# Performance work log

Measured on AMD Instinct MI355X. Metric: run time of the kernel, lower is better.

## Reference

```python
import jax, jax.numpy as jnp
import numpy as np

N, D, K = 131072, 256, 16      # samples, ambient dim, projection dims
NDOM, B, G = 8, 32, 100        # domains, hist_bins, barycenter grid size


def setup_inputs() -> dict:
    key = jax.random.key(0)
    k1, k2, k3, k4, k5, k6 = jax.random.split(key, 6)
    X = jax.random.normal(k1, (N, D), jnp.float32)
    y = jax.random.randint(k2, (N,), 0, NDOM)
    # wT: orthonormal columns via QR with sign fix (as in INB.__init__)
    wi = np.asarray(jax.random.normal(k3, (D, K), jnp.float32))
    Q, R = np.linalg.qr(wi)
    wT = jnp.asarray(Q * np.sign(np.diag(R)), jnp.float32)
    # Per-(domain, dim) histogram bin edges (sorted -> monotone) and CDF values in [0,1]
    bin_edges = jnp.sort(jax.random.normal(k4, (NDOM, K, B + 1), jnp.float32) * 2.0, axis=-1)
    steps = jax.random.uniform(k5, (NDOM, K, B), jnp.float32, minval=0.1, maxval=1.0)
    c = jnp.cumsum(steps, axis=-1)
    cdf_vals = jnp.concatenate([jnp.zeros((NDOM, K, 1), jnp.float32), c / c[..., -1:]], axis=-1)
    # Barycenter inverse-CDF (quantile function) sampled on a uniform grid over [0,1]
    bary_q = jnp.sort(jax.random.normal(k6, (K, G), jnp.float32) * 2.0, axis=-1)
    return {"X": X, "y": y, "wT": wT, "bin_edges": bin_edges,
            "cdf_vals": cdf_vals, "bary_q": bary_q}


def _searchsorted_2d(edges, x):
    # edges: (N, K, B+1) per-sample monotone edges; x: (N, K)
    ss = jax.vmap(jax.vmap(lambda e, v: jnp.searchsorted(e, v, side='right')))(edges, x)
    return jnp.clip(ss - 1, 0, B - 1)  # (N, K) int, left bin index


def reference(X, y, wT, bin_edges, cdf_vals, bary_q):
    Xm = X @ wT                         # (N, K) small-K GEMM
    remaining = X - Xm @ wT.T           # (N, D)
    # gather per-sample domain tables (irregular, data-dependent access)
    eb = bin_edges[y]                   # (N, K, B+1)
    cb = cdf_vals[y]                    # (N, K, B+1)
    i = _searchsorted_2d(eb, Xm)        # (N, K)
    x0 = jnp.take_along_axis(eb, i[..., None], axis=-1)[..., 0]
    x1 = jnp.take_along_axis(eb, i[..., None] + 1, axis=-1)[..., 0]
    f0 = jnp.take_along_axis(cb, i[..., None], axis=-1)[..., 0]
    f1 = jnp.take_along_axis(cb, i[..., None] + 1, axis=-1)[..., 0]
    t = jnp.clip((Xm - x0) / (x1 - x0), 0.0, 1.0)
    u = f0 + t * (f1 - f0)              # per-domain CDF value in [0,1]
    # barycenter inverse CDF: linear interp on uniform grid over [0,1]
    pos = jnp.clip(u, 0.0, 1.0) * (G - 1)
    j = jnp.clip(pos.astype(jnp.int32), 0, G - 2)
    tt = pos - j.astype(pos.dtype)
    kk = jnp.arange(K)[None, :]
    z = bary_q[kk, j] * (1.0 - tt) + bary_q[kk, j + 1] * tt  # (N, K)
    return remaining + z @ wT.T
```

## Files before the change

kernel.cpp:

```cpp
#include <hip/hip_runtime.h>

typedef float v2f __attribute__((ext_vector_type(2)));
typedef float v4f __attribute__((ext_vector_type(4)));

#define N_ROWS 131072
#define DIM    256
#define KP     16
#define NDOM   8
#define NB     32
#define GG     100

#define EB_N   (NDOM*KP*(NB+1))
#define BARY_N (KP*GG)

#define GRID   1536
#define WAVES  4
#define NWAVE  (GRID*WAVES)
#define ITERS  22

__device__ __forceinline__ void pk_fma(v2f &d, v2f a, v2f b) {
    asm("v_pk_fma_f32 %0, %1, %2, %0" : "+v"(d) : "v"(a), "v"(b));
}
__device__ __forceinline__ void pl32swap(float &a, float &b) {
    asm("v_permlane32_swap_b32 %0, %1" : "+v"(a), "+v"(b));
}
__device__ __forceinline__ void pl16swap(float &a, float &b) {
    asm("v_permlane16_swap_b32 %0, %1" : "+v"(a), "+v"(b));
}
__device__ __forceinline__ v2f swap32_sum(v2f lo, v2f hi) {
    float a0 = lo[0], b0 = hi[0], a1 = lo[1], b1 = hi[1];
    pl32swap(a0, b0); pl32swap(a1, b1);
    v2f r; r[0] = a0 + b0; r[1] = a1 + b1; return r;
}
__device__ __forceinline__ v2f swap16_sum(v2f lo, v2f hi) {
    float a0 = lo[0], b0 = hi[0], a1 = lo[1], b1 = hi[1];
    pl16swap(a0, b0); pl16swap(a1, b1);
    v2f r; r[0] = a0 + b0; r[1] = a1 + b1; return r;
}
template <int CODE>
__device__ __forceinline__ float swzf(float x) {
    return __builtin_bit_cast(float,
        __builtin_amdgcn_ds_swizzle(__builtin_bit_cast(int, x), CODE));
}
template <int M>
__device__ __forceinline__ void xor_sum2(v2f &a, v2f &b) {
    constexpr int CODE = (M << 10) | 0x1F;
    a[0] += swzf<CODE>(a[0]); a[1] += swzf<CODE>(a[1]);
    b[0] += swzf<CODE>(b[0]); b[1] += swzf<CODE>(b[1]);
}
__device__ __forceinline__ void wave_fence() {
    asm volatile("s_waitcnt lgkmcnt(0)" ::: "memory");
    __builtin_amdgcn_sched_barrier(0);
}

__global__ __launch_bounds__(256, 4)
void inb_kernel(const float* __restrict__ X, const int* __restrict__ y,
                const float* __restrict__ wT, const float* __restrict__ be,
                const float* __restrict__ cv, const float* __restrict__ bq,
                float* __restrict__ out)
{
    __shared__ float sEB[EB_N];
    __shared__ float sBARY[BARY_N];
    __shared__ float sCOEFF[WAVES][16];

    const int tid = threadIdx.x;
    for (int i = tid; i < EB_N; i += 256) sEB[i] = be[i];
    for (int i = tid; i < BARY_N; i += 256) sBARY[i] = bq[i];
    __syncthreads();

    const int lane = tid & 63;
    const int wid  = tid >> 6;
    const int k      = ((lane & 48) >> 2) | (lane & 3);
    const int echunk = (lane >> 2) & 3;

    v2f wTo[4][8];
#pragma unroll
    for (int j = 0; j < 4; ++j) {
        const v4f* wrow = reinterpret_cast<const v4f*>(&wT[(4*lane + j)*KP]);
#pragma unroll
        for (int q = 0; q < 4; ++q) {
            v4f v = wrow[q];
            v2f a; a[0] = v[0]; a[1] = v[1]; wTo[j][2*q]   = a;
            v2f b; b[0] = v[2]; b[1] = v[3]; wTo[j][2*q+1] = b;
        }
    }

    float* cobuf = sCOEFF[wid];
    const int gwave = blockIdx.x * WAVES + wid;

    v4f x_cur = *reinterpret_cast<const v4f*>(&X[(size_t)gwave*DIM + 4*lane]);
    int pr1 = (gwave + NWAVE < N_ROWS) ? gwave + NWAVE : gwave;
    v4f x_nxt = *reinterpret_cast<const v4f*>(&X[(size_t)pr1*DIM + 4*lane]);
    int dom_cur = y[gwave];

    for (int it = 0; it < ITERS; ++it) {
        const int row = gwave + it*NWAVE;
        if (row >= N_ROWS) break;

        const float* ebRow = &sEB[(dom_cur*KP + k)*(NB+1)];
        float e[8];
#pragma unroll
        for (int t = 0; t < 8; ++t) e[t] = ebRow[8*echunk + t];

        int nr  = row + NWAVE;   if (nr  >= N_ROWS) nr  = row;
        int pfr = row + 2*NWAVE; if (pfr >= N_ROWS) pfr = row;
        int dom_nxt = y[nr];
        v4f x_pf = *reinterpret_cast<const v4f*>(&X[(size_t)pfr*DIM + 4*lane]);

        v2f P[8];
#pragma unroll
        for (int q = 0; q < 8; ++q) { P[q][0] = 0.f; P[q][1] = 0.f; }
#pragma unroll
        for (int j = 0; j < 4; ++j) {
            v2f xj; xj[0] = x_cur[j]; xj[1] = x_cur[j];
#pragma unroll
            for (int q = 0; q < 8; ++q) pk_fma(P[q], xj, wTo[j][q]);
        }

        v2f Q[4];
#pragma unroll
        for (int r = 0; r < 4; ++r)
            Q[r] = swap32_sum(P[r], P[r+4]);
        v2f S0 = swap16_sum(Q[0], Q[2]);
        v2f S1 = swap16_sum(Q[1], Q[3]);
        xor_sum2<8>(S0, S1);
        xor_sum2<4>(S0, S1);
        xor_sum2<2>(S0, S1);
        xor_sum2<1>(S0, S1);
        v2f T = (lane & 2) ? S1 : S0;
        const float xm = (lane & 1) ? T[1] : T[0];

        int cnt = (e[0] <= xm) + (e[1] <= xm) + (e[2] <= xm) + (e[3] <= xm)
                + (e[4] <= xm) + (e[5] <= xm) + (e[6] <= xm) + (e[7] <= xm);
        cnt += __builtin_amdgcn_ds_swizzle(cnt, 0x101F);
        cnt += __builtin_amdgcn_ds_swizzle(cnt, 0x201F);
        int i0 = min(max(cnt - 1, 0), NB - 1);

        float x0 = ebRow[i0], x1 = ebRow[i0+1];
        const float* cfRow = cv + (size_t)(dom_cur*KP + k)*(NB+1);
        float f0 = cfRow[i0], f1 = cfRow[i0+1];

        float t  = fminf(fmaxf(__fdividef(xm - x0, x1 - x0), 0.f), 1.f);
        float u  = f0 + t * (f1 - f0);
        float posv = fminf(fmaxf(u, 0.f), 1.f) * (float)(GG - 1);
        int jj = min((int)posv, GG - 2);
        float ttf = posv - (float)jj;
        float b0 = sBARY[k*GG + jj], b1 = sBARY[k*GG + jj + 1];
        float z = b0*(1.f - ttf) + b1*ttf;
        float coeff = xm - z;

        if ((lane & 12) == 0) cobuf[k] = coeff;
        wave_fence();

        v2f c2[8];
#pragma unroll
        for (int q = 0; q < 4; ++q) {
            v4f cv4 = *reinterpret_cast<const v4f*>(&cobuf[4*q]);
            v2f a; a[0] = cv4[0]; a[1] = cv4[1]; c2[2*q]   = a;
            v2f b; b[0] = cv4[2]; b[1] = cv4[3]; c2[2*q+1] = b;
        }
        float od[4];
#pragma unroll
        for (int j = 0; j < 4; ++j) {
            v2f a = {0.f,0.f};
#pragma unroll
            for (int q = 0; q < 8; ++q) pk_fma(a, c2[q], wTo[j][q]);
            od[j] = x_cur[j] - (a[0] + a[1]);
        }
        v4f o4; o4[0] = od[0]; o4[1] = od[1]; o4[2] = od[2]; o4[3] = od[3];
        *reinterpret_cast<v4f*>(&out[(size_t)row*DIM + 4*lane]) = o4;

        x_cur = x_nxt; x_nxt = x_pf; dom_cur = dom_nxt;
    }
}

extern "C" void kernel_launch(void* const* d_in, const int* in_sizes, int n_in,
                              void* d_out, int out_size, void* d_ws, size_t ws_size,
                              hipStream_t stream) {
    const float* X  = (const float*)d_in[0];
    const int*   y  = (const int*)  d_in[1];
    const float* wT = (const float*)d_in[2];
    const float* be = (const float*)d_in[3];
    const float* cv = (const float*)d_in[4];
    const float* bq = (const float*)d_in[5];
    float* out = (float*)d_out;
    hipLaunchKernelGGL(inb_kernel, dim3(GRID), dim3(256), 0, stream,
                       X, y, wT, be, cv, bq, out);
}
```

Baseline: 81.53 us.

## Process two rows per wave iteration with DPP reductions and LDS-cached CDF table

Result: faster. 71.10 us (-12.8%).

```diff
diff --git a/kernel.cpp b/kernel.cpp
--- a/kernel.cpp
+++ b/kernel.cpp
@@ -13,10 +13,10 @@
 #define EB_N   (NDOM*KP*(NB+1))
 #define BARY_N (KP*GG)
 
-#define GRID   1536
+#define GRID   1024
 #define WAVES  4
 #define NWAVE  (GRID*WAVES)
-#define ITERS  22
+#define PAIRS  16
 
 __device__ __forceinline__ void pk_fma(v2f &d, v2f a, v2f b) {
     asm("v_pk_fma_f32 %0, %1, %2, %0" : "+v"(d) : "v"(a), "v"(b));
@@ -37,20 +37,79 @@
     pl16swap(a0, b0); pl16swap(a1, b1);
     v2f r; r[0] = a0 + b0; r[1] = a1 + b1; return r;
 }
-template <int CODE>
-__device__ __forceinline__ float swzf(float x) {
-    return __builtin_bit_cast(float,
-        __builtin_amdgcn_ds_swizzle(__builtin_bit_cast(int, x), CODE));
-}
-template <int M>
-__device__ __forceinline__ void xor_sum2(v2f &a, v2f &b) {
-    constexpr int CODE = (M << 10) | 0x1F;
-    a[0] += swzf<CODE>(a[0]); a[1] += swzf<CODE>(a[1]);
-    b[0] += swzf<CODE>(b[0]); b[1] += swzf<CODE>(b[1]);
+template <int CTRL>
+__device__ __forceinline__ float dppf(float x) {
+    return __builtin_bit_cast(float, __builtin_amdgcn_update_dpp(
+        0, __builtin_bit_cast(int, x), CTRL, 0xF, 0xF, true));
+}
+template <int CTRL>
+__device__ __forceinline__ int dppi(int x) {
+    return __builtin_amdgcn_update_dpp(0, x, CTRL, 0xF, 0xF, true);
+}
+__device__ __forceinline__ float red16(float v) {
+    v += dppf<0xB1>(v);
+    v += dppf<0x4E>(v);
+    v += dppf<0x141>(v);
+    v += dppf<0x140>(v);
+    return v;
 }
 __device__ __forceinline__ void wave_fence() {
     asm volatile("s_waitcnt lgkmcnt(0)" ::: "memory");
     __builtin_amdgcn_sched_barrier(0);
+}
+
+__device__ __forceinline__ float reduce_scatter(v2f P[8], int lane) {
+    v2f Q[4];
+#pragma unroll
+    for (int r = 0; r < 4; ++r)
+        Q[r] = swap32_sum(P[r], P[r+4]);
+    v2f S0 = swap16_sum(Q[0], Q[2]);
+    v2f S1 = swap16_sum(Q[1], Q[3]);
+    float a = red16(S0[0]), b = red16(S0[1]);
+    float c = red16(S1[0]), d = red16(S1[1]);
+    float lo = (lane & 1) ? b : a;
+    float hi = (lane & 1) ? d : c;
+    return (lane & 2) ? hi : lo;
+}
+
+__device__ __forceinline__ float quantile_map(float xm, const float* ebRow,
+                                              const float* cfRow, const float* bqk,
+                                              const float e[8]) {
+    int cnt = (e[0] <= xm) + (e[1] <= xm) + (e[2] <= xm) + (e[3] <= xm)
+            + (e[4] <= xm) + (e[5] <= xm) + (e[6] <= xm) + (e[7] <= xm);
+    cnt += dppi<0x124>(cnt);
+    cnt += dppi<0x128>(cnt);
+    int i0 = min(max(cnt - 1, 0), NB - 1);
+    float x0 = ebRow[i0], x1 = ebRow[i0+1];
+    float f0 = cfRow[i0], f1 = cfRow[i0+1];
+    float t  = fminf(fmaxf(__fdividef(xm - x0, x1 - x0), 0.f), 1.f);
+    float u  = f0 + t * (f1 - f0);
+    float posv = fminf(fmaxf(u, 0.f), 1.f) * (float)(GG - 1);
+    int jj = min((int)posv, GG - 2);
+    float ttf = posv - (float)jj;
+    float b0 = bqk[jj], b1 = bqk[jj+1];
+    return xm - (b0*(1.f - ttf) + b1*ttf);
+}
+
+__device__ __forceinline__ void out_row(v4f x, const float* cb, v2f (*wTo)[8],
+                                        float* op) {
+    v2f c2[8];
+#pragma unroll
+    for (int q = 0; q < 4; ++q) {
+        v4f cv4 = *reinterpret_cast<const v4f*>(&cb[4*q]);
+        v2f a; a[0] = cv4[0]; a[1] = cv4[1]; c2[2*q]   = a;
+        v2f b; b[0] = cv4[2]; b[1] = cv4[3]; c2[2*q+1] = b;
+    }
+    float od[4];
+#pragma unroll
+    for (int j = 0; j < 4; ++j) {
+        v2f a = {0.f, 0.f};
+#pragma unroll
+        for (int q = 0; q < 8; ++q) pk_fma(a, c2[q], wTo[j][q]);
+        od[j] = x[j] - (a[0] + a[1]);
+    }
+    v4f o4; o4[0] = od[0]; o4[1] = od[1]; o4[2] = od[2]; o4[3] = od[3];
+    *reinterpret_cast<v4f*>(op) = o4;
 }
 
 __global__ __launch_bounds__(256, 4)
@@ -59,19 +118,20 @@
                 const float* __restrict__ cv, const float* __restrict__ bq,
                 float* __restrict__ out)
 {
-    __shared__ float sEB[EB_N];
-    __shared__ float sBARY[BARY_N];
-    __shared__ float sCOEFF[WAVES][16];
+    __shared__ alignas(16) float sEB[EB_N];
+    __shared__ alignas(16) float sCDF[EB_N];
+    __shared__ alignas(16) float sBARY[BARY_N];
+    __shared__ alignas(16) float sCOEFF[WAVES][32];
 
     const int tid = threadIdx.x;
-    for (int i = tid; i < EB_N; i += 256) sEB[i] = be[i];
+    for (int i = tid; i < EB_N; i += 256) { sEB[i] = be[i]; sCDF[i] = cv[i]; }
     for (int i = tid; i < BARY_N; i += 256) sBARY[i] = bq[i];
     __syncthreads();
 
     const int lane = tid & 63;
     const int wid  = tid >> 6;
-    const int k      = ((lane & 48) >> 2) | (lane & 3);
-    const int echunk = (lane >> 2) & 3;
+    const int k  = ((lane & 48) >> 2) | (lane & 3);
+    const int ec = (lane >> 2) & 3;
 
     v2f wTo[4][8];
 #pragma unroll
@@ -87,90 +147,55 @@
 
     float* cobuf = sCOEFF[wid];
     const int gwave = blockIdx.x * WAVES + wid;
-
-    v4f x_cur = *reinterpret_cast<const v4f*>(&X[(size_t)gwave*DIM + 4*lane]);
-    int pr1 = (gwave + NWAVE < N_ROWS) ? gwave + NWAVE : gwave;
-    v4f x_nxt = *reinterpret_cast<const v4f*>(&X[(size_t)pr1*DIM + 4*lane]);
-    int dom_cur = y[gwave];
-
-    for (int it = 0; it < ITERS; ++it) {
-        const int row = gwave + it*NWAVE;
-        if (row >= N_ROWS) break;
-
-        const float* ebRow = &sEB[(dom_cur*KP + k)*(NB+1)];
-        float e[8];
-#pragma unroll
-        for (int t = 0; t < 8; ++t) e[t] = ebRow[8*echunk + t];
-
-        int nr  = row + NWAVE;   if (nr  >= N_ROWS) nr  = row;
-        int pfr = row + 2*NWAVE; if (pfr >= N_ROWS) pfr = row;
-        int dom_nxt = y[nr];
-        v4f x_pf = *reinterpret_cast<const v4f*>(&X[(size_t)pfr*DIM + 4*lane]);
-
-        v2f P[8];
-#pragma unroll
-        for (int q = 0; q < 8; ++q) { P[q][0] = 0.f; P[q][1] = 0.f; }
+    const int xoff  = 4*lane;
+
+    v4f xA = *reinterpret_cast<const v4f*>(&X[(size_t)gwave*DIM + xoff]);
+    v4f xB = *reinterpret_cast<const v4f*>(&X[(size_t)(gwave + NWAVE)*DIM + xoff]);
+    int dA = y[gwave], dB = y[gwave + NWAVE];
+
+    for (int it = 0; it < PAIRS; ++it) {
+        const int rA = gwave + (2*it)*NWAVE;
+        const int rB = rA + NWAVE;
+
+        const float* ebA = &sEB[(dA*KP + k)*(NB+1)];
+        const float* ebB = &sEB[(dB*KP + k)*(NB+1)];
+        float eA[8], eB[8];
+#pragma unroll
+        for (int t = 0; t < 8; ++t) { eA[t] = ebA[8*ec + t]; eB[t] = ebB[8*ec + t]; }
+
+        int nA = rA + 2*NWAVE; if (nA >= N_ROWS) nA = rA;
+        int nB = nA + NWAVE;   if (nB >= N_ROWS) nB = rA;
+        int dA_n = y[nA], dB_n = y[nB];
+        v4f xA_n = *reinterpret_cast<const v4f*>(&X[(size_t)nA*DIM + xoff]);
+        v4f xB_n = *reinterpret_cast<const v4f*>(&X[(size_t)nB*DIM + xoff]);
+
+        v2f PA[8], PB[8];
+#pragma unroll
+        for (int q = 0; q < 8; ++q) { PA[q] = (v2f){0.f,0.f}; PB[q] = (v2f){0.f,0.f}; }
 #pragma unroll
         for (int j = 0; j < 4; ++j) {
-            v2f xj; xj[0] = x_cur[j]; xj[1] = x_cur[j];
-#pragma unroll
-            for (int q = 0; q < 8; ++q) pk_fma(P[q], xj, wTo[j][q]);
+            v2f aj; aj[0] = xA[j]; aj[1] = xA[j];
+            v2f bj; bj[0] = xB[j]; bj[1] = xB[j];
+#pragma unroll
+            for (int q = 0; q < 8; ++q) {
+                pk_fma(PA[q], aj, wTo[j][q]);
+                pk_fma(PB[q], bj, wTo[j][q]);
+            }
         }
 
-        v2f Q[4];
-#pragma unroll
-        for (int r = 0; r < 4; ++r)
-            Q[r] = swap32_sum(P[r], P[r+4]);
-        v2f S0 = swap16_sum(Q[0], Q[2]);
-        v2f S1 = swap16_sum(Q[1], Q[3]);
-        xor_sum2<8>(S0, S1);
-        xor_sum2<4>(S0, S1);
-        xor_sum2<2>(S0, S1);
-        xor_sum2<1>(S0, S1);
-        v2f T = (lane & 2) ? S1 : S0;
-        const float xm = (lane & 1) ? T[1] : T[0];
-
-        int cnt = (e[0] <= xm) + (e[1] <= xm) + (e[2] <= xm) + (e[3] <= xm)
-                + (e[4] <= xm) + (e[5] <= xm) + (e[6] <= xm) + (e[7] <= xm);
-        cnt += __builtin_amdgcn_ds_swizzle(cnt, 0x101F);
-        cnt += __builtin_amdgcn_ds_swizzle(cnt, 0x201F);
-        int i0 = min(max(cnt - 1, 0), NB - 1);
-
-        float x0 = ebRow[i0], x1 = ebRow[i0+1];
-        const float* cfRow = cv + (size_t)(dom_cur*KP + k)*(NB+1);
-        float f0 = cfRow[i0], f1 = cfRow[i0+1];
-
-        float t  = fminf(fmaxf(__fdividef(xm - x0, x1 - x0), 0.f), 1.f);
-        float u  = f0 + t * (f1 - f0);
-        float posv = fminf(fmaxf(u, 0.f), 1.f) * (float)(GG - 1);
-        int jj = min((int)posv, GG - 2);
-        float ttf = posv - (float)jj;
-        float b0 = sBARY[k*GG + jj], b1 = sBARY[k*GG + jj + 1];
-        float z = b0*(1.f - ttf) + b1*ttf;
-        float coeff = xm - z;
-
-        if ((lane & 12) == 0) cobuf[k] = coeff;
+        float xmA = reduce_scatter(PA, lane);
+        float xmB = reduce_scatter(PB, lane);
+
+        float cA = quantile_map(xmA, ebA, &sCDF[(dA*KP + k)*(NB+1)], &sBARY[k*GG], eA);
+        float cB = quantile_map(xmB, ebB, &sCDF[(dB*KP + k)*(NB+1)], &sBARY[k*GG], eB);
+
+        if (ec < 2) cobuf[ec*16 + k] = (ec == 0) ? cA : cB;
         wave_fence();
 
-        v2f c2[8];
-#pragma unroll
-        for (int q = 0; q < 4; ++q) {
-            v4f cv4 = *reinterpret_cast<const v4f*>(&cobuf[4*q]);
-            v2f a; a[0] = cv4[0]; a[1] = cv4[1]; c2[2*q]   = a;
-            v2f b; b[0] = cv4[2]; b[1] = cv4[3]; c2[2*q+1] = b;
-        }
-        float od[4];
-#pragma unroll
-        for (int j = 0; j < 4; ++j) {
-            v2f a = {0.f,0.f};
-#pragma unroll
-            for (int q = 0; q < 8; ++q) pk_fma(a, c2[q], wTo[j][q]);
-            od[j] = x_cur[j] - (a[0] + a[1]);
-        }
-        v4f o4; o4[0] = od[0]; o4[1] = od[1]; o4[2] = od[2]; o4[3] = od[3];
-        *reinterpret_cast<v4f*>(&out[(size_t)row*DIM + 4*lane]) = o4;
-
-        x_cur = x_nxt; x_nxt = x_pf; dom_cur = dom_nxt;
+        out_row(xA, cobuf,      wTo, &out[(size_t)rA*DIM + xoff]);
+        out_row(xB, cobuf + 16, wTo, &out[(size_t)rB*DIM + xoff]);
+
+        xA = xA_n; xB = xB_n; dA = dA_n; dB = dB_n;
     }
 }
 
```
